# Kernel tuning notes

Measured on AMD Instinct MI355X. Metric: run time of the kernel, lower is better.

## Reference

```python
import jax, jax.numpy as jnp
import numpy as np

N_NODES = 50000
N_EDGES = 400000
IN_NODE = 16
OUT_NODE = 20
IN_EDGE = 10
HIDDEN_EDGE = 64
HIDDEN_ACTOR = 256
N_ACTIONS = 16
N_GRAPHS = 128
BN_EPS = 1e-5


def setup_inputs() -> dict:
    key = jax.random.key(0)
    ks = jax.random.split(key, 16)
    inp = {
        "x": jax.random.normal(ks[0], (N_NODES, IN_NODE), dtype=jnp.float32),
        "edge_index": jax.random.randint(ks[1], (2, N_EDGES), 0, N_NODES, dtype=jnp.int64),
        "edge_attr": jax.random.normal(ks[2], (N_EDGES, IN_EDGE), dtype=jnp.float32),
        "batch": jnp.sort(jax.random.randint(ks[3], (N_NODES,), 0, N_GRAPHS, dtype=jnp.int64)),
        # edge-nn params: Lin(in_edge,64) -> BN(64) -> ReLU -> Lin(64, in*out)
        "W1": jax.random.normal(ks[4], (IN_EDGE, HIDDEN_EDGE), dtype=jnp.float32) / np.sqrt(IN_EDGE),
        "b1": jnp.zeros((HIDDEN_EDGE,), dtype=jnp.float32),
        "gamma": jnp.ones((HIDDEN_EDGE,), dtype=jnp.float32),
        "beta": jnp.zeros((HIDDEN_EDGE,), dtype=jnp.float32),
        "W2": jax.random.normal(ks[5], (HIDDEN_EDGE, IN_NODE * OUT_NODE), dtype=jnp.float32) / np.sqrt(HIDDEN_EDGE),
        "b2": jnp.zeros((IN_NODE * OUT_NODE,), dtype=jnp.float32),
        # NNConv root weight + bias
        "root": jax.random.normal(ks[6], (IN_NODE, OUT_NODE), dtype=jnp.float32) / np.sqrt(IN_NODE),
        "bias": jnp.zeros((OUT_NODE,), dtype=jnp.float32),
        # actor MLP: Lin(20,256) -> ReLU -> Lin(256, n_actions)
        "A1": jax.random.normal(ks[7], (OUT_NODE, HIDDEN_ACTOR), dtype=jnp.float32) / np.sqrt(OUT_NODE),
        "ab1": jnp.zeros((HIDDEN_ACTOR,), dtype=jnp.float32),
        "A2": jax.random.normal(ks[8], (HIDDEN_ACTOR, N_ACTIONS), dtype=jnp.float32) / np.sqrt(HIDDEN_ACTOR),
        "ab2": jnp.zeros((N_ACTIONS,), dtype=jnp.float32),
    }
    return inp


def reference(x, edge_index, edge_attr, batch, W1, b1, gamma, beta, W2, b2, root, bias, A1, ab1, A2, ab2):
    # edge nn: Linear -> BatchNorm1d (training-mode batch stats) -> ReLU -> Linear
    h = edge_attr @ W1 + b1                                  # [E, 64]
    mu = jnp.mean(h, axis=0)
    var = jnp.mean((h - mu) ** 2, axis=0)                    # biased var, as BN uses
    h = gamma * (h - mu) * jax.lax.rsqrt(var + BN_EPS) + beta
    h = jax.nn.relu(h)
    w = (h @ W2 + b2).reshape(-1, IN_NODE, OUT_NODE)         # [E, in, out]

    src, dst = edge_index[0], edge_index[1]
    msg = jnp.einsum('ei,eio->eo', x[src], w)                # per-edge matvec, [E, out]
    agg = jax.ops.segment_sum(msg, dst, num_segments=N_NODES)  # scatter-add to targets
    out = agg + x @ root + bias                              # [N, out]

    # global_mean_pool over graphs
    sums = jax.ops.segment_sum(out, batch, num_segments=N_GRAPHS)
    counts = jax.ops.segment_sum(jnp.ones((out.shape[0],), out.dtype), batch, num_segments=N_GRAPHS)
    pooled = sums / jnp.maximum(counts, 1.0)[:, None]        # [G, out]

    a = jax.nn.relu(pooled @ A1 + ab1)
    return a @ A2 + ab2                                      # [G, n_actions]
```

## Files before the change

### kernel.cpp

```cpp
#include <hip/hip_runtime.h>

#define N_NODES   50000
#define N_EDGES   400000
#define IN_NODE   16
#define OUT_NODE  20
#define IN_EDGE   10
#define HE        64
#define HA        256
#define N_ACT     16
#define N_GRAPHS  128
#define BN_EPS    1e-5f
#define HNST      68
#define SPLIT     16

typedef __attribute__((ext_vector_type(8))) short short8v;
typedef __attribute__((ext_vector_type(4))) float f32x4;

__device__ __forceinline__ unsigned short f2bf(float f) {
  unsigned u = __float_as_uint(f);
  u += 0x7fffu + ((u >> 16) & 1u);
  return (unsigned short)(u >> 16);
}
__device__ __forceinline__ float bf2f(short s) {
  return __uint_as_float(((unsigned)(unsigned short)s) << 16);
}

#define DPP_ROR_ADD(v, CTRL)                                                  \
  ((v) + __int_as_float(__builtin_amdgcn_update_dpp(                          \
             0, __float_as_int(v), (CTRL), 0xF, 0xF, true)))
#define ROW_SUM16(v)                                                          \
  do {                                                                        \
    v = DPP_ROR_ADD(v, 0x128);                                                \
    v = DPP_ROR_ADD(v, 0x124);                                                \
    v = DPP_ROR_ADD(v, 0x122);                                                \
    v = DPP_ROR_ADD(v, 0x121);                                                \
  } while (0)

__global__ __launch_bounds__(256) void prep_k(const float* __restrict__ ea,
                                              const int* __restrict__ ei,
                                              const int* __restrict__ batch,
                                              float* __restrict__ hdr,
                                              int* __restrict__ ge,
                                              int* __restrict__ hist) {
  __shared__ float red[4][72];
  __shared__ int lh[N_GRAPHS];
  float cs[10];
  float gm[55];
#pragma unroll
  for (int a = 0; a < 10; ++a) cs[a] = 0.f;
#pragma unroll
  for (int u = 0; u < 55; ++u) gm[u] = 0.f;
  for (int t = threadIdx.x; t < N_GRAPHS; t += 256) lh[t] = 0;
  __syncthreads();

  for (int e = blockIdx.x * 256 + threadIdx.x; e < N_EDGES; e += 256 * 256) {
    const int g = batch[ei[N_EDGES + e]];
    ge[e] = g;
    atomicAdd(&lh[g], 1);
    const float2* rp = reinterpret_cast<const float2*>(ea + (size_t)e * 10);
    float f[10];
#pragma unroll
    for (int p = 0; p < 5; ++p) {
      const float2 t = rp[p];
      f[2 * p] = t.x;
      f[2 * p + 1] = t.y;
    }
#pragma unroll
    for (int a = 0; a < 10; ++a) cs[a] += f[a];
    int idx = 0;
#pragma unroll
    for (int a = 0; a < 10; ++a)
#pragma unroll
      for (int b = a; b < 10; ++b) {
        gm[idx] = fmaf(f[a], f[b], gm[idx]);
        ++idx;
      }
  }

#pragma unroll
  for (int v = 0; v < 10; ++v)
#pragma unroll
    for (int off = 1; off < 64; off <<= 1) cs[v] += __shfl_xor(cs[v], off, 64);
#pragma unroll
  for (int u = 0; u < 55; ++u)
#pragma unroll
    for (int off = 1; off < 64; off <<= 1) gm[u] += __shfl_xor(gm[u], off, 64);

  const int lane = threadIdx.x & 63;
  const int w = threadIdx.x >> 6;
  if (lane == 0) {
#pragma unroll
    for (int v = 0; v < 10; ++v) red[w][v] = cs[v];
#pragma unroll
    for (int u = 0; u < 55; ++u) red[w][10 + u] = gm[u];
  }
  __syncthreads();
  if (threadIdx.x < 65) {
    const int t = threadIdx.x;
    const float s = red[0][t] + red[1][t] + red[2][t] + red[3][t];
    const int dst = (t < 10) ? t : 6 + t;
    atomicAdd(&hdr[dst], s);
  }
  if (threadIdx.x < N_GRAPHS && lh[threadIdx.x] > 0)
    atomicAdd(&hist[threadIdx.x], lh[threadIdx.x]);
}

__global__ void scan_fin_k(const int* __restrict__ hist,
                           int* __restrict__ bstart, int* __restrict__ cursor,
                           const float* __restrict__ hdr,
                           const float* __restrict__ W1,
                           const float* __restrict__ b1,
                           const float* __restrict__ gamma,
                           const float* __restrict__ beta,
                           float* __restrict__ scale,
                           float* __restrict__ c1out) {
  __shared__ int v[N_GRAPHS];
  const int t = threadIdx.x;
  const int h = hist[t];
  v[t] = h;
  __syncthreads();
  for (int off = 1; off < N_GRAPHS; off <<= 1) {
    int y = 0;
    if (t >= off) y = v[t - off];
    __syncthreads();
    v[t] += y;
    __syncthreads();
  }
  bstart[t] = v[t] - h;
  cursor[t] = v[t] - h;
  if (t == N_GRAPHS - 1) bstart[N_GRAPHS] = v[t];

  if (t < HE) {
    const int c = t;
    float wc[10];
#pragma unroll
    for (int k = 0; k < 10; ++k) wc[k] = W1[k * HE + c];
    float su = 0.f;
#pragma unroll
    for (int k = 0; k < 10; ++k) su = fmaf(hdr[k], wc[k], su);
    float q = 0.f;
    int idx = 0;
#pragma unroll
    for (int a = 0; a < 10; ++a) {
      q = fmaf(hdr[16 + idx], wc[a] * wc[a], q);
      ++idx;
#pragma unroll
      for (int b = a + 1; b < 10; ++b) {
        q = fmaf(2.f * hdr[16 + idx], wc[a] * wc[b], q);
        ++idx;
      }
    }
    const float b1c = b1[c];
    const float invE = 1.f / (float)N_EDGES;
    const float mu = su * invE + b1c;
    const float Eh2 = (q + 2.f * b1c * su) * invE + b1c * b1c;
    const float var = Eh2 - mu * mu;
    const float sc = gamma[c] * rsqrtf(var + BN_EPS);
    scale[c] = sc;
    c1out[c] = sc * (b1c - mu) + beta[c];
  }
}

__global__ __launch_bounds__(256) void scatter_k(const int* __restrict__ ge,
                                                 const int* __restrict__ ei,
                                                 int* __restrict__ cursor,
                                                 int* __restrict__ perm,
                                                 int* __restrict__ psrc) {
  __shared__ int lh[N_GRAPHS];
  __shared__ int gb[N_GRAPHS];
  for (int t = threadIdx.x; t < N_GRAPHS; t += 256) lh[t] = 0;
  __syncthreads();
  int gj[7], lr[7], ej[7];
#pragma unroll
  for (int j = 0; j < 7; ++j) {
    const int e = blockIdx.x * 256 + threadIdx.x + j * 65536;
    ej[j] = e;
    gj[j] = -1;
    lr[j] = 0;
    if (e < N_EDGES) {
      const int g = ge[e];
      gj[j] = g;
      lr[j] = atomicAdd(&lh[g], 1);
    }
  }
  __syncthreads();
  if (threadIdx.x < N_GRAPHS && lh[threadIdx.x] > 0)
    gb[threadIdx.x] = atomicAdd(&cursor[threadIdx.x], lh[threadIdx.x]);
  __syncthreads();
#pragma unroll
  for (int j = 0; j < 7; ++j)
    if (gj[j] >= 0) {
      const int pos = gb[gj[j]] + lr[j];
      perm[pos] = ej[j];
      psrc[pos] = ei[ej[j]];
    }
}

__global__ __launch_bounds__(256) void s_kernel(
    const float* __restrict__ x, const float* __restrict__ ea,
    const float* __restrict__ W1g, const float* __restrict__ W2g,
    const float* __restrict__ b2g, const float* __restrict__ scale,
    const float* __restrict__ c1g, const int* __restrict__ perm,
    const int* __restrict__ psrc, const int* __restrict__ bstart,
    float* __restrict__ MSGpart) {
  __shared__ short hnT[2][64 * HNST];
  __shared__ short xT[2][16 * HNST];
  __shared__ float mred[4][OUT_NODE];

  const int tid = threadIdx.x;
  const int lane = tid & 63;
  const int w = tid >> 6;
  const int i_col = lane & 15;
  const int kq = lane >> 4;

  const int g = blockIdx.x / SPLIT;
  const int pp = blockIdx.x - g * SPLIT;
  const int gs = bstart[g], geE = bstart[g + 1];
  const int cnt = geE - gs;
  const int p0 = gs + (cnt * pp) / SPLIT;
  const int p1 = gs + (cnt * (pp + 1)) / SPLIT;

  short8v w1f[4];
  float scv[4], c1v[4];
#pragma unroll
  for (int nt = 0; nt < 4; ++nt) {
    short8v v;
#pragma unroll
    for (int j = 0; j < 8; ++j) {
      const int k = kq * 8 + j;
      const float f = (k < IN_EDGE) ? W1g[k * HE + nt * 16 + i_col] : 0.f;
      v[j] = (short)f2bf(f);
    }
    w1f[nt] = v;
    scv[nt] = scale[nt * 16 + i_col];
    c1v[nt] = c1g[nt * 16 + i_col];
  }

  f32x4 acc = {0.f, 0.f, 0.f, 0.f};
  float xs = 0.f;

  int p = 0;
  for (int base = p0; base < p1; base += 64) {
    {
      const int er = base + w * 16 + i_col;
      const bool val = er < p1;
      const int pe = val ? perm[er] : 0;
      const float* row = ea + (size_t)pe * IN_EDGE;
      float af[8];
#pragma unroll
      for (int j = 0; j < 8; ++j) af[j] = 0.f;
      if (val) {
#pragma unroll
        for (int pr = 0; pr < 4; ++pr) {
          const int k = kq * 8 + pr * 2;
          if (k < IN_EDGE) {
            const float2 t2 = *reinterpret_cast<const float2*>(row + k);
            af[pr * 2] = t2.x;
            af[pr * 2 + 1] = t2.y;
          }
        }
      }
      short8v ae;
#pragma unroll
      for (int j = 0; j < 8; ++j) ae[j] = (short)f2bf(af[j]);

      const f32x4 zero4 = {0.f, 0.f, 0.f, 0.f};
#pragma unroll
      for (int nt = 0; nt < 4; ++nt) {
        const f32x4 hv = __builtin_amdgcn_mfma_f32_16x16x32_bf16(
            ae, w1f[nt], zero4, 0, 0, 0);
        short4 sv;
        {
          const int e0 = base + w * 16 + kq * 4;
          const float h0 = (e0 + 0 < p1) ? fmaxf(fmaf(hv[0], scv[nt], c1v[nt]), 0.f) : 0.f;
          const float h1 = (e0 + 1 < p1) ? fmaxf(fmaf(hv[1], scv[nt], c1v[nt]), 0.f) : 0.f;
          const float h2 = (e0 + 2 < p1) ? fmaxf(fmaf(hv[2], scv[nt], c1v[nt]), 0.f) : 0.f;
          const float h3 = (e0 + 3 < p1) ? fmaxf(fmaf(hv[3], scv[nt], c1v[nt]), 0.f) : 0.f;
          sv.x = (short)f2bf(h0);
          sv.y = (short)f2bf(h1);
          sv.z = (short)f2bf(h2);
          sv.w = (short)f2bf(h3);
        }
        *reinterpret_cast<short4*>(
            &hnT[p][(nt * 16 + i_col) * HNST + w * 16 + kq * 4]) = sv;
      }
    }
    {
      const int et = tid >> 2, iq = tid & 3;
      const int er = base + et;
      float4 xv = {0.f, 0.f, 0.f, 0.f};
      if (er < p1) {
        const int s = psrc[er];
        xv = *reinterpret_cast<const float4*>(&x[(size_t)s * IN_NODE + iq * 4]);
      }
      xT[p][(iq * 4 + 0) * HNST + et] = (short)f2bf(xv.x);
      xT[p][(iq * 4 + 1) * HNST + et] = (short)f2bf(xv.y);
      xT[p][(iq * 4 + 2) * HNST + et] = (short)f2bf(xv.z);
      xT[p][(iq * 4 + 3) * HNST + et] = (short)f2bf(xv.w);
    }
    __syncthreads();
#pragma unroll
    for (int ks = 0; ks < 2; ++ks) {
      const short8v a = *reinterpret_cast<const short8v*>(
          &hnT[p][(w * 16 + i_col) * HNST + ks * 32 + kq * 8]);
      const short8v b = *reinterpret_cast<const short8v*>(
          &xT[p][i_col * HNST + ks * 32 + kq * 8]);
      acc = __builtin_amdgcn_mfma_f32_16x16x32_bf16(a, b, acc, 0, 0, 0);
      if (w == 0) {
#pragma unroll
        for (int j = 0; j < 8; ++j) xs += bf2f(b[j]);
      }
    }
    p ^= 1;
  }

  if (w == 0) {
    xs += __shfl_xor(xs, 16, 64);
    xs += __shfl_xor(xs, 32, 64);
  }
  float po[OUT_NODE];
#pragma unroll
  for (int o = 0; o < OUT_NODE; ++o) po[o] = 0.f;
#pragma unroll
  for (int r = 0; r < 4; ++r) {
    const float* w2p =
        &W2g[(size_t)(w * 16 + kq * 4 + r) * (IN_NODE * OUT_NODE) +
             i_col * OUT_NODE];
#pragma unroll
    for (int o = 0; o < OUT_NODE; ++o) po[o] = fmaf(acc[r], w2p[o], po[o]);
  }
  if (w == 0 && kq == 0) {
    const float* b2p = &b2g[i_col * OUT_NODE];
#pragma unroll
    for (int o = 0; o < OUT_NODE; ++o) po[o] = fmaf(xs, b2p[o], po[o]);
  }
#pragma unroll
  for (int o = 0; o < OUT_NODE; ++o) {
    float s = po[o];
    ROW_SUM16(s);
    s += __shfl_xor(s, 16, 64);
    s += __shfl_xor(s, 32, 64);
    po[o] = s;
  }
  if (lane == 0) {
#pragma unroll
    for (int o = 0; o < OUT_NODE; ++o) mred[w][o] = po[o];
  }
  __syncthreads();
  if (tid < OUT_NODE)
    MSGpart[(size_t)blockIdx.x * OUT_NODE + tid] =
        mred[0][tid] + mred[1][tid] + mred[2][tid] + mred[3][tid];
}

__global__ __launch_bounds__(256) void xsum_k(const float* __restrict__ x,
                                              const int* __restrict__ batch,
                                              float* __restrict__ XN,
                                              float* __restrict__ cnt) {
  __shared__ float xn_l[N_GRAPHS * IN_NODE];
  __shared__ float cnt_l[N_GRAPHS];
  const int tid = threadIdx.x;
  const int lane = tid & 63;
  for (int t = tid; t < N_GRAPHS * IN_NODE; t += 256) xn_l[t] = 0.f;
  if (tid < N_GRAPHS) cnt_l[tid] = 0.f;
  __syncthreads();

  const int n = blockIdx.x * 256 + tid;
  const bool valid = n < N_NODES;
  int g = -1;
  float xf[IN_NODE];
  if (valid) {
    g = batch[n];
    const float4* xp = reinterpret_cast<const float4*>(&x[(size_t)n * IN_NODE]);
    const float4 a0 = xp[0], a1 = xp[1], a2 = xp[2], a3 = xp[3];
    xf[0] = a0.x;  xf[1] = a0.y;  xf[2] = a0.z;  xf[3] = a0.w;
    xf[4] = a1.x;  xf[5] = a1.y;  xf[6] = a1.z;  xf[7] = a1.w;
    xf[8] = a2.x;  xf[9] = a2.y;  xf[10] = a2.z; xf[11] = a2.w;
    xf[12] = a3.x; xf[13] = a3.y; xf[14] = a3.z; xf[15] = a3.w;
  } else {
#pragma unroll
    for (int i = 0; i < IN_NODE; ++i) xf[i] = 0.f;
  }

  const int g0 = __builtin_amdgcn_readfirstlane(g);
  const bool uni = (__ballot(valid && (g == g0)) == 0xFFFFFFFFFFFFFFFFull);

  if (uni) {
#pragma unroll
    for (int i = 0; i < IN_NODE; ++i) {
      float s = xf[i];
      ROW_SUM16(s);
      s += __shfl_xor(s, 16, 64);
      s += __shfl_xor(s, 32, 64);
      xf[i] = s;
    }
    if (lane == 0) {
#pragma unroll
      for (int i = 0; i < IN_NODE; ++i) atomicAdd(&xn_l[g0 * IN_NODE + i], xf[i]);
      atomicAdd(&cnt_l[g0], 64.f);
    }
  } else if (valid) {
#pragma unroll
    for (int i = 0; i < IN_NODE; ++i) atomicAdd(&xn_l[g * IN_NODE + i], xf[i]);
    atomicAdd(&cnt_l[g], 1.f);
  }
  __syncthreads();

  if (tid < N_GRAPHS && cnt_l[tid] != 0.f) atomicAdd(&cnt[tid], cnt_l[tid]);
  for (int t = tid; t < N_GRAPHS * IN_NODE; t += 256) {
    const float v = xn_l[t];
    if (v != 0.f) atomicAdd(&XN[t], v);
  }
}

__global__ __launch_bounds__(256) void fuse_k(
    const float* __restrict__ MSGpart, const float* __restrict__ XN,
    const float* __restrict__ cnt, const float* __restrict__ rootg,
    const float* __restrict__ biasg, const float* __restrict__ A1,
    const float* __restrict__ ab1, const float* __restrict__ A2,
    const float* __restrict__ ab2, float* __restrict__ out) {
  __shared__ float pooled[OUT_NODE];
  __shared__ float a_s[HA];
  __shared__ float red[16][N_ACT];

  const int g = blockIdx.x;
  const int tid = threadIdx.x;
  if (tid < OUT_NODE) {
    float s = 0.f;
#pragma unroll
    for (int q = 0; q < SPLIT; ++q)
      s += MSGpart[(size_t)(g * SPLIT + q) * OUT_NODE + tid];
#pragma unroll
    for (int i = 0; i < IN_NODE; ++i)
      s = fmaf(XN[g * IN_NODE + i], rootg[i * OUT_NODE + tid], s);
    const float invc = 1.f / fmaxf(cnt[g], 1.f);
    pooled[tid] = s * invc + biasg[tid];
  }
  __syncthreads();

  {
    float v = ab1[tid];
#pragma unroll
    for (int k = 0; k < OUT_NODE; ++k) v = fmaf(pooled[k], A1[k * HA + tid], v);
    a_s[tid] = fmaxf(v, 0.f);
  }
  __syncthreads();
  {
    const int j = tid & 15, seg = tid >> 4;
    float v = 0.f;
#pragma unroll
    for (int kk = 0; kk < 16; ++kk) {
      const int k = seg * 16 + kk;
      v += a_s[k] * A2[k * N_ACT + j];
    }
    red[seg][j] = v;
  }
  __syncthreads();
  if (tid < N_ACT) {
    float s = ab2[tid];
#pragma unroll
    for (int seg = 0; seg < 16; ++seg) s += red[seg][tid];
    out[g * N_ACT + tid] = s;
  }
}

extern "C" void kernel_launch(void* const* d_in, const int* in_sizes, int n_in,
                              void* d_out, int out_size, void* d_ws,
                              size_t ws_size, hipStream_t stream) {
  const float* x     = (const float*)d_in[0];
  const int*   ei    = (const int*)d_in[1];
  const float* ea    = (const float*)d_in[2];
  const int*   batch = (const int*)d_in[3];
  const float* W1    = (const float*)d_in[4];
  const float* b1    = (const float*)d_in[5];
  const float* gamma = (const float*)d_in[6];
  const float* beta  = (const float*)d_in[7];
  const float* W2    = (const float*)d_in[8];
  const float* b2    = (const float*)d_in[9];
  const float* root  = (const float*)d_in[10];
  const float* bias  = (const float*)d_in[11];
  const float* A1    = (const float*)d_in[12];
  const float* ab1   = (const float*)d_in[13];
  const float* A2    = (const float*)d_in[14];
  const float* ab2   = (const float*)d_in[15];
  float* out = (float*)d_out;

  float* ws = (float*)d_ws;
  int*   iw = (int*)d_ws;
  float* hdr     = ws;
  float* scale   = ws + 128;
  float* c1      = ws + 192;
  float* XN      = ws + 256;
  float* cntb    = ws + 2304;
  int*   hist    = iw + 2432;
  int*   bstart  = iw + 2560;
  int*   cursor  = iw + 2696;
  int*   ge      = iw + 2824;
  int*   perm    = iw + 402824;
  int*   psrc    = iw + 802824;
  float* MSGpart = ws + 1202824;

  hipMemsetAsync(d_ws, 0, 2560 * sizeof(float), stream);

  prep_k<<<256, 256, 0, stream>>>(ea, ei, batch, hdr, ge, hist);
  scan_fin_k<<<1, 128, 0, stream>>>(hist, bstart, cursor, hdr, W1, b1, gamma,
                                    beta, scale, c1);
  scatter_k<<<256, 256, 0, stream>>>(ge, ei, cursor, perm, psrc);
  s_kernel<<<N_GRAPHS * SPLIT, 256, 0, stream>>>(x, ea, W1, W2, b2, scale, c1,
                                                 perm, psrc, bstart, MSGpart);
  xsum_k<<<(N_NODES + 255) / 256, 256, 0, stream>>>(x, batch, XN, cntb);
  fuse_k<<<N_GRAPHS, 256, 0, stream>>>(MSGpart, XN, cntb, root, bias, A1, ab1,
                                       A2, ab2, out);
}
```

Before: 86.88 us.

## Pack sorted bf16 edge attributes and source features in scatter pass

The scatter kernel now gathers edge attributes and source node features and writes them as a packed bf16 64-byte record at the graph-sorted position. It also accumulates the BatchNorm moment statistics, which moves them out of prep_k. The main kernel then reads contiguous packed records instead of indirecting through perm/psrc into ea and x, and it computes the BN scale and shift itself in shared memory. The memset is replaced by a small zeroing kernel, and launch bounds request two blocks per CU. In exchange, the 12.8 MB intermediate must be written and read back, and the BN finalisation is repeated in every block.

```diff
diff --git a/kernel.cpp b/kernel.cpp
--- a/kernel.cpp
+++ b/kernel.cpp
@@ -36,84 +36,25 @@
     v = DPP_ROR_ADD(v, 0x121);                                                \
   } while (0)
 
-__global__ __launch_bounds__(256) void prep_k(const float* __restrict__ ea,
-                                              const int* __restrict__ ei,
+__global__ void zero_k(float* __restrict__ ws) {
+  ws[blockIdx.x * 256 + threadIdx.x] = 0.f;
+}
+
+__global__ __launch_bounds__(256) void prep_k(const int* __restrict__ ei,
                                               const int* __restrict__ batch,
-                                              float* __restrict__ hdr,
-                                              int* __restrict__ ge,
                                               int* __restrict__ hist) {
-  __shared__ float red[4][72];
   __shared__ int lh[N_GRAPHS];
-  float cs[10];
-  float gm[55];
-#pragma unroll
-  for (int a = 0; a < 10; ++a) cs[a] = 0.f;
-#pragma unroll
-  for (int u = 0; u < 55; ++u) gm[u] = 0.f;
-  for (int t = threadIdx.x; t < N_GRAPHS; t += 256) lh[t] = 0;
-  __syncthreads();
-
-  for (int e = blockIdx.x * 256 + threadIdx.x; e < N_EDGES; e += 256 * 256) {
-    const int g = batch[ei[N_EDGES + e]];
-    ge[e] = g;
-    atomicAdd(&lh[g], 1);
-    const float2* rp = reinterpret_cast<const float2*>(ea + (size_t)e * 10);
-    float f[10];
-#pragma unroll
-    for (int p = 0; p < 5; ++p) {
-      const float2 t = rp[p];
-      f[2 * p] = t.x;
-      f[2 * p + 1] = t.y;
-    }
-#pragma unroll
-    for (int a = 0; a < 10; ++a) cs[a] += f[a];
-    int idx = 0;
-#pragma unroll
-    for (int a = 0; a < 10; ++a)
-#pragma unroll
-      for (int b = a; b < 10; ++b) {
-        gm[idx] = fmaf(f[a], f[b], gm[idx]);
-        ++idx;
-      }
-  }
-
-#pragma unroll
-  for (int v = 0; v < 10; ++v)
-#pragma unroll
-    for (int off = 1; off < 64; off <<= 1) cs[v] += __shfl_xor(cs[v], off, 64);
-#pragma unroll
-  for (int u = 0; u < 55; ++u)
-#pragma unroll
-    for (int off = 1; off < 64; off <<= 1) gm[u] += __shfl_xor(gm[u], off, 64);
-
-  const int lane = threadIdx.x & 63;
-  const int w = threadIdx.x >> 6;
-  if (lane == 0) {
-#pragma unroll
-    for (int v = 0; v < 10; ++v) red[w][v] = cs[v];
-#pragma unroll
-    for (int u = 0; u < 55; ++u) red[w][10 + u] = gm[u];
-  }
-  __syncthreads();
-  if (threadIdx.x < 65) {
-    const int t = threadIdx.x;
-    const float s = red[0][t] + red[1][t] + red[2][t] + red[3][t];
-    const int dst = (t < 10) ? t : 6 + t;
-    atomicAdd(&hdr[dst], s);
-  }
-  if (threadIdx.x < N_GRAPHS && lh[threadIdx.x] > 0)
-    atomicAdd(&hist[threadIdx.x], lh[threadIdx.x]);
-}
-
-__global__ void scan_fin_k(const int* __restrict__ hist,
-                           int* __restrict__ bstart, int* __restrict__ cursor,
-                           const float* __restrict__ hdr,
-                           const float* __restrict__ W1,
-                           const float* __restrict__ b1,
-                           const float* __restrict__ gamma,
-                           const float* __restrict__ beta,
-                           float* __restrict__ scale,
-                           float* __restrict__ c1out) {
+  const int tid = threadIdx.x;
+  if (tid < N_GRAPHS) lh[tid] = 0;
+  __syncthreads();
+  for (int e = blockIdx.x * 256 + tid; e < N_EDGES; e += 256 * 256)
+    atomicAdd(&lh[batch[ei[N_EDGES + e]]], 1);
+  __syncthreads();
+  if (tid < N_GRAPHS && lh[tid] > 0) atomicAdd(&hist[tid], lh[tid]);
+}
+
+__global__ void scan_k(const int* __restrict__ hist, int* __restrict__ bstart,
+                       int* __restrict__ cursor) {
   __shared__ int v[N_GRAPHS];
   const int t = threadIdx.x;
   const int h = hist[t];
@@ -129,12 +70,138 @@
   bstart[t] = v[t] - h;
   cursor[t] = v[t] - h;
   if (t == N_GRAPHS - 1) bstart[N_GRAPHS] = v[t];
-
-  if (t < HE) {
-    const int c = t;
+}
+
+__global__ __launch_bounds__(256) void scatter_k(
+    const float* __restrict__ ea, const int* __restrict__ ei,
+    const int* __restrict__ batch, const float* __restrict__ x,
+    int* __restrict__ cursor, unsigned short* __restrict__ exb,
+    float* __restrict__ hdr) {
+  __shared__ int lh[N_GRAPHS];
+  __shared__ int gb[N_GRAPHS];
+  __shared__ float red[4][72];
+  const int tid = threadIdx.x;
+
+  float cs[10];
+  float gm[55];
+#pragma unroll
+  for (int a = 0; a < 10; ++a) cs[a] = 0.f;
+#pragma unroll
+  for (int u = 0; u < 55; ++u) gm[u] = 0.f;
+  if (tid < N_GRAPHS) lh[tid] = 0;
+  __syncthreads();
+
+  int gj[7], lr[7];
+#pragma unroll
+  for (int j = 0; j < 7; ++j) {
+    const int e = blockIdx.x * 256 + tid + j * 65536;
+    gj[j] = -1;
+    lr[j] = 0;
+    if (e < N_EDGES) {
+      const int g = batch[ei[N_EDGES + e]];
+      gj[j] = g;
+      lr[j] = atomicAdd(&lh[g], 1);
+    }
+  }
+  __syncthreads();
+  if (tid < N_GRAPHS && lh[tid] > 0)
+    gb[tid] = atomicAdd(&cursor[tid], lh[tid]);
+  __syncthreads();
+
+#pragma unroll
+  for (int j = 0; j < 7; ++j) {
+    if (gj[j] < 0) continue;
+    const int e = blockIdx.x * 256 + tid + j * 65536;
+    const float2* rp = reinterpret_cast<const float2*>(ea + (size_t)e * 10);
+    float f[10];
+#pragma unroll
+    for (int p = 0; p < 5; ++p) {
+      const float2 t2 = rp[p];
+      f[2 * p] = t2.x;
+      f[2 * p + 1] = t2.y;
+    }
+#pragma unroll
+    for (int a = 0; a < 10; ++a) cs[a] += f[a];
+    int idx = 0;
+#pragma unroll
+    for (int a = 0; a < 10; ++a)
+#pragma unroll
+      for (int b = a; b < 10; ++b) {
+        gm[idx] = fmaf(f[a], f[b], gm[idx]);
+        ++idx;
+      }
+    const int s = ei[e];
+    const float4* xp = reinterpret_cast<const float4*>(&x[(size_t)s * IN_NODE]);
+    const float4 x0 = xp[0], x1 = xp[1], x2 = xp[2], x3 = xp[3];
+    unsigned u[16];
+    u[0] = f2bf(f[0]) | ((unsigned)f2bf(f[1]) << 16);
+    u[1] = f2bf(f[2]) | ((unsigned)f2bf(f[3]) << 16);
+    u[2] = f2bf(f[4]) | ((unsigned)f2bf(f[5]) << 16);
+    u[3] = f2bf(f[6]) | ((unsigned)f2bf(f[7]) << 16);
+    u[4] = f2bf(f[8]) | ((unsigned)f2bf(f[9]) << 16);
+    u[5] = 0; u[6] = 0; u[7] = 0;
+    u[8]  = f2bf(x0.x) | ((unsigned)f2bf(x0.y) << 16);
+    u[9]  = f2bf(x0.z) | ((unsigned)f2bf(x0.w) << 16);
+    u[10] = f2bf(x1.x) | ((unsigned)f2bf(x1.y) << 16);
+    u[11] = f2bf(x1.z) | ((unsigned)f2bf(x1.w) << 16);
+    u[12] = f2bf(x2.x) | ((unsigned)f2bf(x2.y) << 16);
+    u[13] = f2bf(x2.z) | ((unsigned)f2bf(x2.w) << 16);
+    u[14] = f2bf(x3.x) | ((unsigned)f2bf(x3.y) << 16);
+    u[15] = f2bf(x3.z) | ((unsigned)f2bf(x3.w) << 16);
+    const int pos = gb[gj[j]] + lr[j];
+    int4* dst = reinterpret_cast<int4*>(exb + (size_t)pos * 32);
+    dst[0] = int4{(int)u[0], (int)u[1], (int)u[2], (int)u[3]};
+    dst[1] = int4{(int)u[4], (int)u[5], (int)u[6], (int)u[7]};
+    dst[2] = int4{(int)u[8], (int)u[9], (int)u[10], (int)u[11]};
+    dst[3] = int4{(int)u[12], (int)u[13], (int)u[14], (int)u[15]};
+  }
+
+#pragma unroll
+  for (int v = 0; v < 10; ++v)
+#pragma unroll
+    for (int off = 1; off < 64; off <<= 1) cs[v] += __shfl_xor(cs[v], off, 64);
+#pragma unroll
+  for (int u = 0; u < 55; ++u)
+#pragma unroll
+    for (int off = 1; off < 64; off <<= 1) gm[u] += __shfl_xor(gm[u], off, 64);
+  const int lane = tid & 63;
+  const int w = tid >> 6;
+  if (lane == 0) {
+#pragma unroll
+    for (int v = 0; v < 10; ++v) red[w][v] = cs[v];
+#pragma unroll
+    for (int u = 0; u < 55; ++u) red[w][10 + u] = gm[u];
+  }
+  __syncthreads();
+  if (tid < 65) {
+    const float s = red[0][tid] + red[1][tid] + red[2][tid] + red[3][tid];
+    const int dst = (tid < 10) ? tid : 6 + tid;
+    atomicAdd(&hdr[dst], s);
+  }
+}
+
+__global__ __launch_bounds__(256, 2) void s_kernel(
+    const unsigned short* __restrict__ exb, const float* __restrict__ W1g,
+    const float* __restrict__ W2g, const float* __restrict__ b2g,
+    const float* __restrict__ b1, const float* __restrict__ gamma,
+    const float* __restrict__ beta, const float* __restrict__ hdr,
+    const int* __restrict__ bstart, float* __restrict__ MSGpart) {
+  __shared__ short hnT[2][64 * HNST];
+  __shared__ short xT[2][16 * HNST];
+  __shared__ float mred[4][OUT_NODE];
+  __shared__ float scs[HE], c1s[HE];
+
+  const int tid = threadIdx.x;
+  const int lane = tid & 63;
+  const int w = tid >> 6;
+  const int i_col = lane & 15;
+  const int kq = lane >> 4;
+
+  if (tid < HE) {
+    const int c = tid;
     float wc[10];
 #pragma unroll
-    for (int k = 0; k < 10; ++k) wc[k] = W1[k * HE + c];
+    for (int k = 0; k < 10; ++k) wc[k] = W1g[k * HE + c];
     float su = 0.f;
 #pragma unroll
     for (int k = 0; k < 10; ++k) su = fmaf(hdr[k], wc[k], su);
@@ -156,62 +223,10 @@
     const float Eh2 = (q + 2.f * b1c * su) * invE + b1c * b1c;
     const float var = Eh2 - mu * mu;
     const float sc = gamma[c] * rsqrtf(var + BN_EPS);
-    scale[c] = sc;
-    c1out[c] = sc * (b1c - mu) + beta[c];
-  }
-}
-
-__global__ __launch_bounds__(256) void scatter_k(const int* __restrict__ ge,
-                                                 const int* __restrict__ ei,
-                                                 int* __restrict__ cursor,
-                                                 int* __restrict__ perm,
-                                                 int* __restrict__ psrc) {
-  __shared__ int lh[N_GRAPHS];
-  __shared__ int gb[N_GRAPHS];
-  for (int t = threadIdx.x; t < N_GRAPHS; t += 256) lh[t] = 0;
-  __syncthreads();
-  int gj[7], lr[7], ej[7];
-#pragma unroll
-  for (int j = 0; j < 7; ++j) {
-    const int e = blockIdx.x * 256 + threadIdx.x + j * 65536;
-    ej[j] = e;
-    gj[j] = -1;
-    lr[j] = 0;
-    if (e < N_EDGES) {
-      const int g = ge[e];
-      gj[j] = g;
-      lr[j] = atomicAdd(&lh[g], 1);
-    }
-  }
-  __syncthreads();
-  if (threadIdx.x < N_GRAPHS && lh[threadIdx.x] > 0)
-    gb[threadIdx.x] = atomicAdd(&cursor[threadIdx.x], lh[threadIdx.x]);
-  __syncthreads();
-#pragma unroll
-  for (int j = 0; j < 7; ++j)
-    if (gj[j] >= 0) {
-      const int pos = gb[gj[j]] + lr[j];
-      perm[pos] = ej[j];
-      psrc[pos] = ei[ej[j]];
-    }
-}
-
-__global__ __launch_bounds__(256) void s_kernel(
-    const float* __restrict__ x, const float* __restrict__ ea,
-    const float* __restrict__ W1g, const float* __restrict__ W2g,
-    const float* __restrict__ b2g, const float* __restrict__ scale,
-    const float* __restrict__ c1g, const int* __restrict__ perm,
-    const int* __restrict__ psrc, const int* __restrict__ bstart,
-    float* __restrict__ MSGpart) {
-  __shared__ short hnT[2][64 * HNST];
-  __shared__ short xT[2][16 * HNST];
-  __shared__ float mred[4][OUT_NODE];
-
-  const int tid = threadIdx.x;
-  const int lane = tid & 63;
-  const int w = tid >> 6;
-  const int i_col = lane & 15;
-  const int kq = lane >> 4;
+    scs[c] = sc;
+    c1s[c] = sc * (b1c - mu) + beta[c];
+  }
+  __syncthreads();
 
   const int g = blockIdx.x / SPLIT;
   const int pp = blockIdx.x - g * SPLIT;
@@ -232,8 +247,8 @@
       v[j] = (short)f2bf(f);
     }
     w1f[nt] = v;
-    scv[nt] = scale[nt * 16 + i_col];
-    c1v[nt] = c1g[nt * 16 + i_col];
+    scv[nt] = scs[nt * 16 + i_col];
+    c1v[nt] = c1s[nt * 16 + i_col];
   }
 
   f32x4 acc = {0.f, 0.f, 0.f, 0.f};
@@ -243,27 +258,13 @@
   for (int base = p0; base < p1; base += 64) {
     {
       const int er = base + w * 16 + i_col;
-      const bool val = er < p1;
-      const int pe = val ? perm[er] : 0;
-      const float* row = ea + (size_t)pe * IN_EDGE;
-      float af[8];
-#pragma unroll
-      for (int j = 0; j < 8; ++j) af[j] = 0.f;
-      if (val) {
-#pragma unroll
-        for (int pr = 0; pr < 4; ++pr) {
-          const int k = kq * 8 + pr * 2;
-          if (k < IN_EDGE) {
-            const float2 t2 = *reinterpret_cast<const float2*>(row + k);
-            af[pr * 2] = t2.x;
-            af[pr * 2 + 1] = t2.y;
-          }
-        }
+      short8v ae;
+      if (kq < 2) {
+        ae = *reinterpret_cast<const short8v*>(&exb[(size_t)er * 32 + kq * 8]);
+      } else {
+#pragma unroll
+        for (int j = 0; j < 8; ++j) ae[j] = 0;
       }
-      short8v ae;
-#pragma unroll
-      for (int j = 0; j < 8; ++j) ae[j] = (short)f2bf(af[j]);
-
       const f32x4 zero4 = {0.f, 0.f, 0.f, 0.f};
 #pragma unroll
       for (int nt = 0; nt < 4; ++nt) {
@@ -288,15 +289,14 @@
     {
       const int et = tid >> 2, iq = tid & 3;
       const int er = base + et;
-      float4 xv = {0.f, 0.f, 0.f, 0.f};
-      if (er < p1) {
-        const int s = psrc[er];
-        xv = *reinterpret_cast<const float4*>(&x[(size_t)s * IN_NODE + iq * 4]);
-      }
-      xT[p][(iq * 4 + 0) * HNST + et] = (short)f2bf(xv.x);
-      xT[p][(iq * 4 + 1) * HNST + et] = (short)f2bf(xv.y);
-      xT[p][(iq * 4 + 2) * HNST + et] = (short)f2bf(xv.z);
-      xT[p][(iq * 4 + 3) * HNST + et] = (short)f2bf(xv.w);
+      short4 xv = {0, 0, 0, 0};
+      if (er < p1)
+        xv = *reinterpret_cast<const short4*>(
+            &exb[(size_t)er * 32 + 16 + iq * 4]);
+      xT[p][(iq * 4 + 0) * HNST + et] = xv.x;
+      xT[p][(iq * 4 + 1) * HNST + et] = xv.y;
+      xT[p][(iq * 4 + 2) * HNST + et] = xv.z;
+      xT[p][(iq * 4 + 3) * HNST + et] = xv.w;
     }
     __syncthreads();
 #pragma unroll
@@ -487,26 +487,20 @@
   float* ws = (float*)d_ws;
   int*   iw = (int*)d_ws;
   float* hdr     = ws;
-  float* scale   = ws + 128;
-  float* c1      = ws + 192;
   float* XN      = ws + 256;
   float* cntb    = ws + 2304;
   int*   hist    = iw + 2432;
   int*   bstart  = iw + 2560;
   int*   cursor  = iw + 2696;
-  int*   ge      = iw + 2824;
-  int*   perm    = iw + 402824;
-  int*   psrc    = iw + 802824;
-  float* MSGpart = ws + 1202824;
-
-  hipMemsetAsync(d_ws, 0, 2560 * sizeof(float), stream);
-
-  prep_k<<<256, 256, 0, stream>>>(ea, ei, batch, hdr, ge, hist);
-  scan_fin_k<<<1, 128, 0, stream>>>(hist, bstart, cursor, hdr, W1, b1, gamma,
-                                    beta, scale, c1);
-  scatter_k<<<256, 256, 0, stream>>>(ge, ei, cursor, perm, psrc);
-  s_kernel<<<N_GRAPHS * SPLIT, 256, 0, stream>>>(x, ea, W1, W2, b2, scale, c1,
-                                                 perm, psrc, bstart, MSGpart);
+  float* MSGpart = ws + 2824;
+  unsigned short* exb = (unsigned short*)(iw + 402824);
+
+  zero_k<<<10, 256, 0, stream>>>(ws);
+  prep_k<<<256, 256, 0, stream>>>(ei, batch, hist);
+  scan_k<<<1, 128, 0, stream>>>(hist, bstart, cursor);
+  scatter_k<<<256, 256, 0, stream>>>(ea, ei, batch, x, cursor, exb, hdr);
+  s_kernel<<<N_GRAPHS * SPLIT, 256, 0, stream>>>(exb, W1, W2, b2, b1, gamma,
+                                                 beta, hdr, bstart, MSGpart);
   xsum_k<<<(N_NODES + 255) / 256, 256, 0, stream>>>(x, batch, XN, cntb);
   fuse_k<<<N_GRAPHS, 256, 0, stream>>>(MSGpart, XN, cntb, root, bias, A1, ab1,
                                        A2, ab2, out);
```

Measured after the change: 84.14 us. 3.1% less time.
